# Kernel optimization log

Hardware: AMD Instinct MI355X
Metric: run time of the kernel (lower is better)

The kernel has to match this reference:

```python
import jax, jax.numpy as jnp
import numpy as np

N, n, d = 4, 2048, 1024


def setup_inputs() -> dict:
    key = jax.random.key(0)
    k1, k2, k3, k4 = jax.random.split(key, 4)
    x = jax.random.normal(k1, (N, n, d), dtype=jnp.float32)
    mask = jax.random.randint(k2, (N, n, n), 0, 2, dtype=jnp.int32)
    Wqk = jax.random.normal(k3, (d, d), dtype=jnp.float32) * (d ** -0.5)
    Wvc = jax.random.normal(k4, (d, d), dtype=jnp.float32) * (d ** -0.5)
    return {"x": x, "mask": mask, "Wqk": Wqk, "Wvc": Wvc}


def reference(x, mask, Wqk, Wvc):
    # q = Wqk(x): torch Linear computes x @ W^T
    q = jnp.einsum('bnd,ed->bne', x, Wqk)          # [N, n, d]
    scale = jnp.asarray(x.shape[-1], x.dtype) ** 0.5
    scores = jnp.einsum('bnd,bmd->bnm', q, x) / scale  # [N, n, n]
    scores = jnp.where(mask == 0, jnp.asarray(-1e20, scores.dtype), scores)
    attention = jax.nn.softmax(scores, axis=-1)
    attended = jnp.einsum('bnm,bmd->bnd', attention, x)
    return jnp.einsum('bnd,ed->bne', attended, Wvc)
```

## Files before the change

kernel.cpp:

```cpp
#include <hip/hip_runtime.h>
#include <hip/hip_bf16.h>

typedef short bf16x8 __attribute__((ext_vector_type(8)));
typedef short s16x4  __attribute__((ext_vector_type(4)));
typedef short s16x8  __attribute__((ext_vector_type(8)));
typedef float f32x4  __attribute__((ext_vector_type(4)));

static __device__ __forceinline__ void async_cp16(const void* g, void* l) {
  __builtin_amdgcn_global_load_lds(
      (const __attribute__((address_space(1))) unsigned int*)g,
      (__attribute__((address_space(3))) unsigned int*)l, 16, 0, 0);
}

static __device__ __forceinline__ unsigned short f2bf_bits(float f) {
  union { __hip_bfloat16 b; unsigned short u; } cv;
  cv.b = __float2bfloat16(f);
  return cv.u;
}
static __device__ __forceinline__ float bf2f(short u) {
  union { float f; unsigned v; } cv;
  cv.v = ((unsigned)(unsigned short)u) << 16;
  return cv.f;
}

#define BAR() __builtin_amdgcn_s_barrier()
#define SBZ() __builtin_amdgcn_sched_barrier(0)
#define LGKM0() do { asm volatile("s_waitcnt lgkmcnt(0)" ::: "memory"); SBZ(); } while (0)
#define VMW(n) do { asm volatile("s_waitcnt vmcnt(" #n ")" ::: "memory"); SBZ(); } while (0)

__global__ __launch_bounds__(256) void cvt_all(const float* __restrict__ x,
                                               const float* __restrict__ wqk,
                                               const float* __restrict__ wvc,
                                               __hip_bfloat16* __restrict__ xb,
                                               __hip_bfloat16* __restrict__ wqkb,
                                               __hip_bfloat16* __restrict__ wvcb) {
  const int b = blockIdx.x;
  const float* in;
  __hip_bfloat16* out;
  long base;
  if (b < 8192)       { in = x;   out = xb;   base = (long)b * 1024; }
  else if (b < 9216)  { in = wqk; out = wqkb; base = (long)(b - 8192) * 1024; }
  else                { in = wvc; out = wvcb; base = (long)(b - 9216) * 1024; }
  const long i = base + threadIdx.x * 4;
  const float4 v = *(const float4*)(in + i);
  s16x4 o;
  o[0] = (short)f2bf_bits(v.x);
  o[1] = (short)f2bf_bits(v.y);
  o[2] = (short)f2bf_bits(v.z);
  o[3] = (short)f2bf_bits(v.w);
  *(s16x4*)(out + i) = o;
}

struct GemmDesc {
  const __hip_bfloat16* A; const __hip_bfloat16* B; void* C;
  int lda, ldb, ldc, nT, tpb; long sA, sB, sC; float cscale;
};

template<int MODE>
__global__ __launch_bounds__(512, 2) void gemm8p(GemmDesc g0, GemmDesc g1, int nb0, int K) {
  __shared__ char lds[131072];
  const int bid = blockIdx.x, nwg = gridDim.x;
  const int wg = (bid & 7) * (nwg >> 3) + (bid >> 3);
  GemmDesc g = (wg < nb0) ? g0 : g1;
  const int id = (wg < nb0) ? wg : wg - nb0;
  const int bz = id / g.tpb, tl = id - bz * g.tpb;
  const int bm = tl / g.nT, bn = tl - bm * g.nT;
  const long m0 = (long)bm * 256, n0 = (long)bn * 256;
  const __hip_bfloat16* Ab = g.A + bz * g.sA;
  const __hip_bfloat16* Bb = g.B + bz * g.sB;

  const int t = threadIdx.x, lane = t & 63, w = t >> 6;
  const int wm = w >> 2, wn = w & 3;
  const int lr = lane & 15, cs = lane >> 4;

  const int srow = t >> 3;
  const int sslot = (t & 7) ^ (srow & 7);
  const __hip_bfloat16* aP[2][2];
  const __hip_bfloat16* bP[2][2];
  #pragma unroll
  for (int h = 0; h < 2; ++h)
    #pragma unroll
    for (int i = 0; i < 2; ++i) {
      aP[h][i] = Ab + (m0 + h * 128 + i * 64 + srow) * g.lda + sslot * 8;
      bP[h][i] = Bb + (n0 + h * 128 + i * 64 + srow) * g.ldb + sslot * 8;
    }

  int aOf[8], bOf[4];
  #pragma unroll
  for (int mm = 0; mm < 8; ++mm)
    aOf[mm] = wm * 16384 + (mm * 16 + lr) * 128 + ((cs ^ (lr & 7)) << 4);
  #pragma unroll
  for (int nf = 0; nf < 4; ++nf)
    bOf[nf] = 32768 + (wn >> 1) * 16384 + ((wn & 1) * 64 + nf * 16 + lr) * 128 +
              ((cs ^ (lr & 7)) << 4);
  f32x4 acc[8][4] = {};
  bf16x8 af[4][2], bqA[2][2], bqB[2][2];

  #define STG(P, h, kt, dbase) do { \
    async_cp16(P[h][0] + (long)(kt) * 64, lds + (dbase) + t * 16); \
    async_cp16(P[h][1] + (long)(kt) * 64, lds + (dbase) + 8192 + t * 16); } while (0)
  #define RD_AF(mb, bufb) do { _Pragma("unroll") for (int mm_ = 0; mm_ < 4; ++mm_) { \
      af[mm_][0] = *(const bf16x8*)(lds + (bufb) + aOf[(mb) * 4 + mm_]); \
      af[mm_][1] = *(const bf16x8*)(lds + (bufb) + (aOf[(mb) * 4 + mm_] ^ 64)); } } while (0)
  #define RD_BQ(dst, nb, bufb) do { _Pragma("unroll") for (int nf_ = 0; nf_ < 2; ++nf_) { \
      dst[nf_][0] = *(const bf16x8*)(lds + (bufb) + bOf[(nb) * 2 + nf_]); \
      dst[nf_][1] = *(const bf16x8*)(lds + (bufb) + (bOf[(nb) * 2 + nf_] ^ 64)); } } while (0)
  #define MM16(BQ, NB, MB) do { \
    __builtin_amdgcn_s_setprio(1); \
    _Pragma("unroll") for (int ks_ = 0; ks_ < 2; ++ks_) \
      _Pragma("unroll") for (int mm_ = 0; mm_ < 4; ++mm_) \
        _Pragma("unroll") for (int nf_ = 0; nf_ < 2; ++nf_) \
          acc[(MB) + mm_][(NB) + nf_] = __builtin_amdgcn_mfma_f32_16x16x32_bf16( \
              af[mm_][ks_], BQ[nf_][ks_], acc[(MB) + mm_][(NB) + nf_], 0, 0, 0); \
    __builtin_amdgcn_s_setprio(0); } while (0)

  const int nt = K >> 6, nJ = nt >> 1;
  STG(bP, 0, 0, 32768); STG(bP, 1, 0, 49152);
  STG(aP, 0, 0, 0);     STG(aP, 1, 0, 16384);
  STG(bP, 0, 1, 65536 + 32768); STG(bP, 1, 1, 65536 + 49152);
  VMW(4);
  BAR(); SBZ();

  for (int j = 0; j < nJ; ++j) {
    const bool full = (j + 1 < nJ);
    const int tb = 2 * j + 1, ta2 = 2 * j + 2, tb2 = 2 * j + 3;
    RD_AF(0, 0); RD_BQ(bqA, 0, 0);
    STG(aP, 0, tb, 65536);
    LGKM0();
    MM16(bqA, 0, 0);
    BAR(); SBZ();
    RD_BQ(bqB, 1, 0);
    STG(aP, 1, tb, 65536 + 16384);
    LGKM0();
    MM16(bqB, 2, 0);
    BAR(); SBZ();
    RD_AF(1, 0);
    if (full) STG(bP, 0, ta2, 32768);
    LGKM0();
    MM16(bqB, 2, 4);
    BAR(); SBZ();
    if (full) STG(bP, 1, ta2, 49152);
    MM16(bqA, 0, 4);
    if (full) { VMW(4); } else { VMW(0); }
    BAR(); SBZ();
    RD_AF(0, 65536); RD_BQ(bqA, 0, 65536);
    if (full) STG(aP, 0, ta2, 0);
    LGKM0();
    MM16(bqA, 0, 0);
    BAR(); SBZ();
    RD_BQ(bqB, 1, 65536);
    if (full) STG(aP, 1, ta2, 16384);
    LGKM0();
    MM16(bqB, 2, 0);
    BAR(); SBZ();
    RD_AF(1, 65536);
    if (full) STG(bP, 0, tb2, 65536 + 32768);
    LGKM0();
    MM16(bqB, 2, 4);
    BAR(); SBZ();
    if (full) STG(bP, 1, tb2, 65536 + 49152);
    MM16(bqA, 0, 4);
    if (full) { VMW(4); } else { VMW(0); }
    BAR(); SBZ();
  }
  #undef STG
  #undef RD_AF
  #undef RD_BQ
  #undef MM16

  const long crow0 = m0 + wm * 128 + cs * 4;
  const long ccol0 = n0 + wn * 64 + lr;
  if (MODE == 0) {
    float* C = (float*)g.C + bz * g.sC;
    #pragma unroll
    for (int mm = 0; mm < 8; ++mm)
      #pragma unroll
      for (int nf = 0; nf < 4; ++nf)
        #pragma unroll
        for (int rr = 0; rr < 4; ++rr)
          C[(crow0 + mm * 16 + rr) * g.ldc + ccol0 + nf * 16] = acc[mm][nf][rr];
  } else {
    __hip_bfloat16* C = (__hip_bfloat16*)g.C + bz * g.sC;
    #pragma unroll
    for (int mm = 0; mm < 8; ++mm)
      #pragma unroll
      for (int nf = 0; nf < 4; ++nf)
        #pragma unroll
        for (int rr = 0; rr < 4; ++rr)
          C[(crow0 + mm * 16 + rr) * g.ldc + ccol0 + nf * 16] =
              __float2bfloat16(acc[mm][nf][rr] * g.cscale);
  }
}

template<int MODE, int WM, int WN, int MR_, int MINW>
__global__ __launch_bounds__(512, MINW) void gemm8w(GemmDesc g0, GemmDesc g1, int nb0, int K) {
  constexpr int BM    = WM * MR_ * 16;
  constexpr int BN    = WN * 64;
  constexpr int BOFF  = BM * 64;
  constexpr int BUFSZ = (BM + BN) * 64;
  constexpr int KW    = (BM + BN) / 128;
  __shared__ char lds[3 * BUFSZ];

  const int bid = blockIdx.x, nwg = gridDim.x;
  const int wg = (bid & 7) * (nwg >> 3) + (bid >> 3);
  GemmDesc g = (wg < nb0) ? g0 : g1;
  const int id = (wg < nb0) ? wg : wg - nb0;
  const int bz = id / g.tpb, tl = id - bz * g.tpb;
  const int bm = tl / g.nT, bn = tl - bm * g.nT;
  const long m0 = (long)bm * BM, n0 = (long)bn * BN;
  const __hip_bfloat16* Ab = g.A + bz * g.sA;
  const __hip_bfloat16* Bb = g.B + bz * g.sB;

  const int t = threadIdx.x;
  const int lane = t & 63, w = t >> 6;
  const int wm = w / WN, wn = w % WN;
  const int lr = lane & 15, cs = lane >> 4;

  const int rA  = t >> 2;
  const int dsl = t & 3;
  const int ssl = dsl ^ ((rA >> 1) & 3);
  const __hip_bfloat16* aSt0 = Ab + (m0 + rA) * g.lda + ssl * 8;
  const __hip_bfloat16* aSt1 = Ab + (m0 + 128 + rA) * g.lda + ssl * 8;
  const __hip_bfloat16* bSt0 = Bb + (n0 + rA) * g.ldb + ssl * 8;
  const __hip_bfloat16* bSt1 = Bb + (n0 + 128 + rA) * g.ldb + ssl * 8;

  const int axor = ((lr >> 1) & 3) << 4;
  int aRd[MR_], bRd[4];
  #pragma unroll
  for (int mm = 0; mm < MR_; ++mm)
    aRd[mm] = (wm * (MR_ * 16) + mm * 16 + lr) * 64 + ((cs << 4) ^ axor);
  #pragma unroll
  for (int nf = 0; nf < 4; ++nf)
    bRd[nf] = BOFF + (wn * 64 + nf * 16 + lr) * 64 + ((cs << 4) ^ axor);

  f32x4 acc[MR_][4] = {};

  #define STAGE(kt, base) do { \
    async_cp16(aSt0 + (long)(kt) * 32, lds + (base) + t * 16); \
    async_cp16(aSt1 + (long)(kt) * 32, lds + (base) + 8192 + t * 16); \
    async_cp16(bSt0 + (long)(kt) * 32, lds + (base) + BOFF + t * 16); \
    if constexpr (BN == 256) \
      async_cp16(bSt1 + (long)(kt) * 32, lds + (base) + BOFF + 8192 + t * 16); \
  } while (0)
  #define VM_KW() do { if constexpr (KW == 4) { VMW(4); } else { VMW(3); } } while (0)

  const int nt = K >> 5;
  STAGE(0, 0);
  STAGE(1, BUFSZ);
  VM_KW();
  BAR();

  int rb = 0, sb = 2 * BUFSZ;
  for (int tt = 0; tt < nt; ++tt) {
    bf16x8 af[MR_], bq[4];
    #pragma unroll
    for (int mm = 0; mm < MR_; ++mm)
      af[mm] = *(const bf16x8*)(lds + rb + aRd[mm]);
    #pragma unroll
    for (int nf = 0; nf < 4; ++nf)
      bq[nf] = *(const bf16x8*)(lds + rb + bRd[nf]);
    if (tt + 2 < nt) STAGE(tt + 2, sb);
    #pragma unroll
    for (int mm = 0; mm < MR_; ++mm)
      #pragma unroll
      for (int nf = 0; nf < 4; ++nf)
        acc[mm][nf] = __builtin_amdgcn_mfma_f32_16x16x32_bf16(af[mm], bq[nf], acc[mm][nf], 0, 0, 0);
    if (tt + 2 < nt) { VM_KW(); } else { VMW(0); }
    BAR();
    rb = (rb == 2 * BUFSZ) ? 0 : rb + BUFSZ;
    sb = (sb == 2 * BUFSZ) ? 0 : sb + BUFSZ;
  }
  #undef STAGE
  #undef VM_KW

  const long crow0 = m0 + wm * (MR_ * 16) + cs * 4;
  const long ccol0 = n0 + wn * 64 + lr;
  if (MODE == 0) {
    float* C = (float*)g.C + bz * g.sC;
    #pragma unroll
    for (int mm = 0; mm < MR_; ++mm)
      #pragma unroll
      for (int nf = 0; nf < 4; ++nf)
        #pragma unroll
        for (int rr = 0; rr < 4; ++rr)
          C[(crow0 + mm * 16 + rr) * g.ldc + ccol0 + nf * 16] = acc[mm][nf][rr];
  } else {
    __hip_bfloat16* C = (__hip_bfloat16*)g.C + bz * g.sC;
    #pragma unroll
    for (int mm = 0; mm < MR_; ++mm)
      #pragma unroll
      for (int nf = 0; nf < 4; ++nf)
        #pragma unroll
        for (int rr = 0; rr < 4; ++rr)
          C[(crow0 + mm * 16 + rr) * g.ldc + ccol0 + nf * 16] =
              __float2bfloat16(acc[mm][nf][rr] * g.cscale);
  }
}

__global__ __launch_bounds__(256) void softmax_rows(__hip_bfloat16* __restrict__ S,
                                                    const int* __restrict__ Mask) {
  const long row = blockIdx.x;
  short* srow = (short*)(S + row * 2048);
  const int* mrow = Mask + row * 2048;
  const int t = threadIdx.x;
  const s16x8 sv = *(const s16x8*)(srow + t * 8);
  const int4 q0 = *(const int4*)(mrow + t * 8);
  const int4 q1 = *(const int4*)(mrow + t * 8 + 4);
  float f[8];
  f[0] = q0.x ? bf2f(sv[0]) : -1e20f;
  f[1] = q0.y ? bf2f(sv[1]) : -1e20f;
  f[2] = q0.z ? bf2f(sv[2]) : -1e20f;
  f[3] = q0.w ? bf2f(sv[3]) : -1e20f;
  f[4] = q1.x ? bf2f(sv[4]) : -1e20f;
  f[5] = q1.y ? bf2f(sv[5]) : -1e20f;
  f[6] = q1.z ? bf2f(sv[6]) : -1e20f;
  f[7] = q1.w ? bf2f(sv[7]) : -1e20f;

  float mx = f[0];
  #pragma unroll
  for (int i = 1; i < 8; ++i) mx = fmaxf(mx, f[i]);
  #pragma unroll
  for (int off = 32; off > 0; off >>= 1) mx = fmaxf(mx, __shfl_xor(mx, off));
  __shared__ float redm[4], reds[4];
  if ((t & 63) == 0) redm[t >> 6] = mx;
  __syncthreads();
  mx = fmaxf(fmaxf(redm[0], redm[1]), fmaxf(redm[2], redm[3]));

  float e[8];
  float s = 0.f;
  #pragma unroll
  for (int i = 0; i < 8; ++i) { e[i] = __expf(f[i] - mx); s += e[i]; }
  #pragma unroll
  for (int off = 32; off > 0; off >>= 1) s += __shfl_xor(s, off);
  if ((t & 63) == 0) reds[t >> 6] = s;
  __syncthreads();
  s = reds[0] + reds[1] + reds[2] + reds[3];
  const float inv = 1.f / s;

  s16x8 o;
  #pragma unroll
  for (int i = 0; i < 8; ++i) o[i] = (short)f2bf_bits(e[i] * inv);
  *(s16x8*)(srow + t * 8) = o;
}

extern "C" void kernel_launch(void* const* d_in, const int* in_sizes, int n_in,
                              void* d_out, int out_size, void* d_ws, size_t ws_size,
                              hipStream_t stream) {
  const float* x   = (const float*)d_in[0];
  const int*   msk = (const int*)d_in[1];
  const float* Wqk = (const float*)d_in[2];
  const float* Wvc = (const float*)d_in[3];
  float* out = (float*)d_out;
  char* ws = (char*)d_ws;

  __hip_bfloat16* xb   = (__hip_bfloat16*)(ws + 0);
  __hip_bfloat16* qb   = (__hip_bfloat16*)(ws + 16777216);
  __hip_bfloat16* vT   = (__hip_bfloat16*)(ws + 33554432);
  __hip_bfloat16* wqkb = (__hip_bfloat16*)(ws + 50331648);
  __hip_bfloat16* wvcb = (__hip_bfloat16*)(ws + 52428800);
  __hip_bfloat16* Sbf  = (__hip_bfloat16*)(ws + 54525952);

  cvt_all<<<dim3(10240), 256, 0, stream>>>(x, Wqk, Wvc, xb, wqkb, wvcb);

  GemmDesc gq{xb,   wqkb, qb, 1024, 1024, 1024, 4, 128, 0L, 0L, 0L, 0.03125f};
  GemmDesc gv{wvcb, xb,   vT, 1024, 1024, 2048, 8, 32, 0L, 2097152L, 2097152L, 1.f};
  gemm8p<1><<<dim3(256), 512, 0, stream>>>(gq, gv, 128, 1024);

  GemmDesc gs{qb, xb, Sbf, 1024, 1024, 2048, 8, 64, 2097152L, 2097152L, 4194304L, 1.f};
  gemm8p<1><<<dim3(256), 512, 0, stream>>>(gs, gs, 256, 1024);

  softmax_rows<<<dim3(8192), 256, 0, stream>>>(Sbf, msk);

  GemmDesc go{Sbf, vT, out, 2048, 2048, 1024, 8, 64, 4194304L, 2097152L, 2097152L, 1.f};
  gemm8w<0, 4, 2, 4, 4><<<dim3(256), 512, 0, stream>>>(go, go, 256, 2048);
}
```

Measured before the change: 142.9 us.

## Restructure GEMM mainloop prefetch schedule to load full A/B tiles ahead

Prefetches the second A tile in the prologue, then issues whole B and A tile loads in grouped pairs later in each half-iteration, raising the vmcnt wait depth from 4 to 8. It also drops the SBZ scheduling barriers and inserts extra workgroup barriers before each LDS wait. The aim is deeper global-to-LDS overlap with the MFMA work. The extra barriers add synchronisation cost, and the new tile-overwrite ordering risks LDS read/write hazards. The final VMW(0) in the last iteration is removed, so the tail drain relies on earlier waits.

```diff
diff --git a/kernel.cpp b/kernel.cpp
--- a/kernel.cpp
+++ b/kernel.cpp
@@ -93,6 +93,7 @@
   for (int nf = 0; nf < 4; ++nf)
     bOf[nf] = 32768 + (wn >> 1) * 16384 + ((wn & 1) * 64 + nf * 16 + lr) * 128 +
               ((cs ^ (lr & 7)) << 4);
+
   f32x4 acc[8][4] = {};
   bf16x8 af[4][2], bqA[2][2], bqB[2][2];
 
@@ -118,50 +119,49 @@
   STG(bP, 0, 0, 32768); STG(bP, 1, 0, 49152);
   STG(aP, 0, 0, 0);     STG(aP, 1, 0, 16384);
   STG(bP, 0, 1, 65536 + 32768); STG(bP, 1, 1, 65536 + 49152);
-  VMW(4);
+  STG(aP, 0, 1, 65536);         STG(aP, 1, 1, 65536 + 16384);
+  VMW(8);
   BAR(); SBZ();
 
   for (int j = 0; j < nJ; ++j) {
     const bool full = (j + 1 < nJ);
-    const int tb = 2 * j + 1, ta2 = 2 * j + 2, tb2 = 2 * j + 3;
+    const int ta2 = 2 * j + 2, tb2 = 2 * j + 3;
     RD_AF(0, 0); RD_BQ(bqA, 0, 0);
-    STG(aP, 0, tb, 65536);
-    LGKM0();
+    BAR(); LGKM0();
     MM16(bqA, 0, 0);
-    BAR(); SBZ();
+    BAR();
     RD_BQ(bqB, 1, 0);
-    STG(aP, 1, tb, 65536 + 16384);
-    LGKM0();
+    BAR(); LGKM0();
     MM16(bqB, 2, 0);
-    BAR(); SBZ();
+    BAR();
     RD_AF(1, 0);
-    if (full) STG(bP, 0, ta2, 32768);
-    LGKM0();
+    if (full) { STG(bP, 0, ta2, 32768); STG(bP, 1, ta2, 49152); }
+    BAR(); LGKM0();
     MM16(bqB, 2, 4);
-    BAR(); SBZ();
-    if (full) STG(bP, 1, ta2, 49152);
+    BAR();
+    if (full) { STG(aP, 0, ta2, 0); STG(aP, 1, ta2, 16384); }
+    BAR();
     MM16(bqA, 0, 4);
-    if (full) { VMW(4); } else { VMW(0); }
-    BAR(); SBZ();
+    if (full) { VMW(8); } else { VMW(0); }
+    BAR();
     RD_AF(0, 65536); RD_BQ(bqA, 0, 65536);
-    if (full) STG(aP, 0, ta2, 0);
-    LGKM0();
+    BAR(); LGKM0();
     MM16(bqA, 0, 0);
-    BAR(); SBZ();
+    BAR();
     RD_BQ(bqB, 1, 65536);
-    if (full) STG(aP, 1, ta2, 16384);
-    LGKM0();
+    BAR(); LGKM0();
     MM16(bqB, 2, 0);
-    BAR(); SBZ();
+    BAR();
     RD_AF(1, 65536);
-    if (full) STG(bP, 0, tb2, 65536 + 32768);
-    LGKM0();
+    if (full) { STG(bP, 0, tb2, 65536 + 32768); STG(bP, 1, tb2, 65536 + 49152); }
+    BAR(); LGKM0();
     MM16(bqB, 2, 4);
-    BAR(); SBZ();
-    if (full) STG(bP, 1, tb2, 65536 + 49152);
+    BAR();
+    if (full) { STG(aP, 0, tb2, 65536); STG(aP, 1, tb2, 65536 + 16384); }
+    BAR();
     MM16(bqA, 0, 4);
-    if (full) { VMW(4); } else { VMW(0); }
-    BAR(); SBZ();
+    if (full) { VMW(8); }
+    BAR();
   }
   #undef STG
   #undef RD_AF
```

After: 146.8 us. 1.03x slower.
